# Performance work log

Measured on AMD Instinct MI355X. Metric: run time of the kernel, lower is better.

The kernel has to match this reference:

```python
import jax, jax.numpy as jnp
import numpy as np

N, T, S = 8192, 512, 4
ND, NC = 8, 16


def setup_inputs() -> dict:
    key = jax.random.key(0)
    ks = jax.random.split(key, 8)
    return {
        "drivers": jax.random.normal(ks[0], (N, T, ND), jnp.float32),
        "covariates": jax.random.normal(ks[1], (N, T, NC), jnp.float32),
        "Y": jax.random.normal(ks[2], (N, T, 1), jnp.float32),
        "eps": jax.random.normal(ks[3], (S, N, T, 1), jnp.float32),
        "tilde_psi": jnp.array([0.5], jnp.float32),
        "gamma_w": jax.random.normal(ks[4], (1, ND), jnp.float32) * 0.1,
        "alpha_w": jax.random.normal(ks[5], (1, NC), jnp.float32) * 0.1,
        "alpha_Y_lag": jnp.array([0.1], jnp.float32),
        "log_tilde_sigma": jnp.array([-1.0], jnp.float32),
        "mu_init": jnp.array([0.0], jnp.float32),
        "log_sigma_init": jnp.array([0.0], jnp.float32),
    }


def reference(drivers, covariates, Y, eps, tilde_psi, gamma_w, alpha_w,
              alpha_Y_lag, log_tilde_sigma, mu_init, log_sigma_init):
    psi = tilde_psi[0]
    sigma = jnp.exp(log_tilde_sigma[0])
    sigma0 = jnp.exp(log_sigma_init[0])

    # Structural drift gamma^T D_t + alpha^T W_t for all t in parallel: (N, T)
    proj = (jnp.einsum('ntd,d->nt', drivers, gamma_w[0])
            + jnp.einsum('ntc,c->nt', covariates, alpha_w[0]))
    # b_t for t>=1 includes lagged-outcome term alpha_Y_lag * Y_{t-1}: (N, T-1)
    b = proj[:, 1:] + alpha_Y_lag[0] * Y[:, :-1, 0]

    # Initial step (use_Y_in_init=False): mu_0 = mu_init + proj_0
    mu0 = mu_init[0] + proj[:, 0]                      # (N,)
    e = eps[..., 0]                                    # (S, N, T)
    Z0 = mu0[None, :] + sigma0 * e[:, :, 0]            # (S, N)

    def step(Z, xs):
        b_t, e_t = xs                                  # (N,), (S, N)
        mu_t = psi * Z + b_t[None, :]
        Z_new = mu_t + sigma * e_t
        return Z_new, (Z_new, mu_t)

    xs = (b.T, jnp.moveaxis(e[:, :, 1:], 2, 0))        # (T-1, N), (T-1, S, N)
    _, (Zs, mus) = jax.lax.scan(step, Z0, xs)          # each (T-1, S, N)

    Z_all = jnp.concatenate([Z0[None], Zs], axis=0)    # (T, S, N)
    mu_all = jnp.concatenate([jnp.broadcast_to(mu0, (S, N))[None], mus], axis=0)

    Z_out = jnp.moveaxis(Z_all, 0, 2)[..., None]       # (S, N, T, 1)
    mu_out = jnp.moveaxis(mu_all, 0, 2)[..., None]

    lv0 = jnp.broadcast_to(2.0 * log_sigma_init[0], (S, N, 1))
    lvt = jnp.broadcast_to(2.0 * log_tilde_sigma[0], (S, N, T - 1))
    lv_out = jnp.concatenate([lv0, lvt], axis=2)[..., None]

    return Z_out, mu_out, lv_out
```

## Files before the change

kernel.cpp:

```cpp
#include <hip/hip_runtime.h>

#define N 8192
#define T 512
#define S 4

__device__ __forceinline__ float dot4(float4 a, float4 b) {
    return a.x*b.x + a.y*b.y + a.z*b.z + a.w*b.w;
}

__global__ __launch_bounds__(256) void k_fused(
        const float* __restrict__ drivers,
        const float* __restrict__ cov,
        const float* __restrict__ Y,
        const float* __restrict__ eps,
        const float* __restrict__ tilde_psi,
        const float* __restrict__ gamma_w,
        const float* __restrict__ alpha_w,
        const float* __restrict__ alpha_Y_lag,
        const float* __restrict__ log_tilde_sigma,
        const float* __restrict__ mu_init,
        const float* __restrict__ log_sigma_init,
        float* __restrict__ Zout,
        float* __restrict__ muout,
        float* __restrict__ lvout) {
    const int n    = blockIdx.x * (blockDim.x >> 6) + (threadIdx.x >> 6);
    const int lane = threadIdx.x & 63;
    const int t0   = lane * 8;

    const float psi    = tilde_psi[0];
    const float lts    = log_tilde_sigma[0];
    const float lsi    = log_sigma_init[0];
    const float sigma  = expf(lts);
    const float sigma0 = expf(lsi);
    const float aY     = alpha_Y_lag[0];

    const float4* g4 = (const float4*)gamma_w;
    const float4* a4 = (const float4*)alpha_w;
    const float4 g0 = g4[0], g1 = g4[1];
    const float4 w0 = a4[0], w1 = a4[1], w2 = a4[2], w3 = a4[3];

    float pj[9];
    pj[0] = 1.f;
    #pragma unroll
    for (int i = 1; i <= 8; ++i) pj[i] = pj[i-1] * psi;
    float wd[6];
    wd[0] = pj[8];
    #pragma unroll
    for (int i = 1; i < 6; ++i) wd[i] = wd[i-1] * wd[i-1];

    const size_t ntbase = (size_t)n * T + t0;
    float b[8];
    {
        float proj[8];
        #pragma unroll
        for (int j = 0; j < 8; ++j) {
            const float4* d4 = (const float4*)(drivers + (ntbase + j) * 8);
            const float4* c4 = (const float4*)(cov     + (ntbase + j) * 16);
            float4 dA = d4[0], dB = d4[1];
            float4 cA = c4[0], cB = c4[1], cC = c4[2], cD = c4[3];
            proj[j] = dot4(dA, g0) + dot4(dB, g1)
                    + dot4(cA, w0) + dot4(cB, w1) + dot4(cC, w2) + dot4(cD, w3);
        }
        const float4* y4 = (const float4*)(Y + ntbase);
        float4 yA = y4[0], yB = y4[1];
        float yprev = __shfl_up(yB.w, 1);
        b[0] = (lane == 0) ? (mu_init[0] + proj[0]) : (proj[0] + aY * yprev);
        b[1] = proj[1] + aY * yA.x;
        b[2] = proj[2] + aY * yA.y;
        b[3] = proj[3] + aY * yA.z;
        b[4] = proj[4] + aY * yA.w;
        b[5] = proj[5] + aY * yB.x;
        b[6] = proj[6] + aY * yB.y;
        b[7] = proj[7] + aY * yB.z;
    }

    const float lvv = 2.f * lts;
    const float4 lB = make_float4(lvv, lvv, lvv, lvv);
    const float4 lA = make_float4(lane == 0 ? 2.f * lsi : lvv, lvv, lvv, lvv);

    #pragma unroll
    for (int s = 0; s < S; ++s) {
        const size_t chain = ((size_t)s * N + n) * T + t0;
        const float4* e4 = (const float4*)(eps + chain);
        float4 eA = e4[0], eB = e4[1];
        float e[8] = {eA.x, eA.y, eA.z, eA.w, eB.x, eB.y, eB.z, eB.w};

        float z[8];
        float acc = 0.f;
        #pragma unroll
        for (int j = 0; j < 8; ++j) {
            float sg = (lane == 0 && j == 0) ? sigma0 : sigma;
            acc = psi * acc + (b[j] + sg * e[j]);
            z[j] = acc;
        }

        float v = acc;
        #pragma unroll
        for (int i = 0, d = 1; d < 64; d <<= 1, ++i) {
            float up = __shfl_up(v, d);
            v += (lane >= d) ? wd[i] * up : 0.f;
        }
        float Zprev = __shfl_up(v, 1);
        Zprev = (lane == 0) ? 0.f : Zprev;

        float Zf[8], mu[8];
        #pragma unroll
        for (int j = 0; j < 8; ++j) {
            Zf[j] = z[j] + pj[j + 1] * Zprev;
            float sg = (lane == 0 && j == 0) ? sigma0 : sigma;
            mu[j] = Zf[j] - sg * e[j];
        }

        float4* z4 = (float4*)(Zout  + chain);
        float4* m4 = (float4*)(muout + chain);
        float4* l4 = (float4*)(lvout + chain);
        z4[0] = make_float4(Zf[0], Zf[1], Zf[2], Zf[3]);
        z4[1] = make_float4(Zf[4], Zf[5], Zf[6], Zf[7]);
        m4[0] = make_float4(mu[0], mu[1], mu[2], mu[3]);
        m4[1] = make_float4(mu[4], mu[5], mu[6], mu[7]);
        l4[0] = lA;
        l4[1] = lB;
    }
}

extern "C" void kernel_launch(void* const* d_in, const int* in_sizes, int n_in,
                              void* d_out, int out_size, void* d_ws, size_t ws_size,
                              hipStream_t stream) {
    const float* drivers   = (const float*)d_in[0];
    const float* cov       = (const float*)d_in[1];
    const float* Y         = (const float*)d_in[2];
    const float* eps       = (const float*)d_in[3];
    const float* tilde_psi = (const float*)d_in[4];
    const float* gamma_w   = (const float*)d_in[5];
    const float* alpha_w   = (const float*)d_in[6];
    const float* aY        = (const float*)d_in[7];
    const float* lts       = (const float*)d_in[8];
    const float* mu_init   = (const float*)d_in[9];
    const float* lsi       = (const float*)d_in[10];

    float* out   = (float*)d_out;
    const size_t SNT = (size_t)S * N * T;
    float* Zout  = out;
    float* muout = out + SNT;
    float* lvout = out + 2 * SNT;

    k_fused<<<N / 4, 256, 0, stream>>>(drivers, cov, Y, eps, tilde_psi,
                                       gamma_w, alpha_w, aY, lts, mu_init, lsi,
                                       Zout, muout, lvout);
}
```

Measured before the change: 154.3 us.

## Stage driver/covariate rows through swizzled LDS and map one wave per sample

Each block now handles a single series n. All 256 threads first load that series' drivers and covariates with fully coalesced float4 reads into XOR-swizzled shared memory, then compute the drift b into shared memory. Each wave then runs one of the S=4 chains as two 256-step segments, doing a wave scan on 4 elements per lane and carrying the tail value between segments. This replaces per-lane strided 8-row loads and removes the duplicated eps/output work per series. In exchange it adds block barriers and shared-memory traffic and launches 4x more blocks.

```diff
diff --git a/kernel.cpp b/kernel.cpp
--- a/kernel.cpp
+++ b/kernel.cpp
@@ -7,6 +7,7 @@
 __device__ __forceinline__ float dot4(float4 a, float4 b) {
     return a.x*b.x + a.y*b.y + a.z*b.z + a.w*b.w;
 }
+__device__ __forceinline__ int swz(int c) { return c ^ ((c >> 3) & 7); }
 
 __global__ __launch_bounds__(256) void k_fused(
         const float* __restrict__ drivers,
@@ -23,9 +24,15 @@
         float* __restrict__ Zout,
         float* __restrict__ muout,
         float* __restrict__ lvout) {
-    const int n    = blockIdx.x * (blockDim.x >> 6) + (threadIdx.x >> 6);
-    const int lane = threadIdx.x & 63;
-    const int t0   = lane * 8;
+    __shared__ float4 dstage[512];
+    __shared__ float4 cstage[1024];
+    __shared__ float4 b_s4[128];
+    float* b_s = (float*)b_s4;
+
+    const int tid  = threadIdx.x;
+    const int lane = tid & 63;
+    const int w    = tid >> 6;
+    const int n    = blockIdx.x;
 
     const float psi    = tilde_psi[0];
     const float lts    = log_tilde_sigma[0];
@@ -33,93 +40,106 @@
     const float sigma  = expf(lts);
     const float sigma0 = expf(lsi);
     const float aY     = alpha_Y_lag[0];
+    const float mu0c   = mu_init[0];
 
     const float4* g4 = (const float4*)gamma_w;
     const float4* a4 = (const float4*)alpha_w;
     const float4 g0 = g4[0], g1 = g4[1];
     const float4 w0 = a4[0], w1 = a4[1], w2 = a4[2], w3 = a4[3];
 
-    float pj[9];
-    pj[0] = 1.f;
+    const size_t chain = ((size_t)w * N + n) * (T / 4);
+    const float4* e4 = (const float4*)eps + chain;
+    const float4 eA = e4[lane];
+    const float4 eB = e4[64 + lane];
+
+    const float4* drv4 = (const float4*)drivers + (size_t)n * (T * 2);
+    const float4* cov4 = (const float4*)cov     + (size_t)n * (T * 4);
+    const float*  Yrow = Y + (size_t)n * T;
+
     #pragma unroll
-    for (int i = 1; i <= 8; ++i) pj[i] = pj[i-1] * psi;
-    float wd[6];
-    wd[0] = pj[8];
-    #pragma unroll
-    for (int i = 1; i < 6; ++i) wd[i] = wd[i-1] * wd[i-1];
+    for (int h = 0; h < 2; ++h) {
+        if (h) __syncthreads();
+        dstage[swz(tid)]       = drv4[h * 512 + tid];
+        dstage[swz(tid + 256)] = drv4[h * 512 + 256 + tid];
+        #pragma unroll
+        for (int k = 0; k < 4; ++k)
+            cstage[swz(tid + 256 * k)] = cov4[h * 1024 + tid + 256 * k];
+        const int t = h * 256 + tid;
+        const float yprev = (t > 0) ? Yrow[t - 1] : 0.f;
+        __syncthreads();
+        const float4 dA = dstage[swz(2 * tid)];
+        const float4 dB = dstage[swz(2 * tid + 1)];
+        const float4 cA = cstage[swz(4 * tid)];
+        const float4 cB = cstage[swz(4 * tid + 1)];
+        const float4 cC = cstage[swz(4 * tid + 2)];
+        const float4 cD = cstage[swz(4 * tid + 3)];
+        const float proj = dot4(dA, g0) + dot4(dB, g1)
+                         + dot4(cA, w0) + dot4(cB, w1)
+                         + dot4(cC, w2) + dot4(cD, w3);
+        b_s[t] = (t == 0) ? (mu0c + proj) : (proj + aY * yprev);
+    }
+    __syncthreads();
 
-    const size_t ntbase = (size_t)n * T + t0;
-    float b[8];
+    const float pj1 = psi, pj2 = psi * psi, pj3 = pj2 * psi, pj4 = pj2 * pj2;
+    const float wd0 = pj4, wd1 = wd0 * wd0, wd2 = wd1 * wd1,
+                wd3 = wd2 * wd2, wd4 = wd3 * wd3, wd5 = wd4 * wd4;
+    float p4l = 1.f;
     {
-        float proj[8];
-        #pragma unroll
-        for (int j = 0; j < 8; ++j) {
-            const float4* d4 = (const float4*)(drivers + (ntbase + j) * 8);
-            const float4* c4 = (const float4*)(cov     + (ntbase + j) * 16);
-            float4 dA = d4[0], dB = d4[1];
-            float4 cA = c4[0], cB = c4[1], cC = c4[2], cD = c4[3];
-            proj[j] = dot4(dA, g0) + dot4(dB, g1)
-                    + dot4(cA, w0) + dot4(cB, w1) + dot4(cC, w2) + dot4(cD, w3);
-        }
-        const float4* y4 = (const float4*)(Y + ntbase);
-        float4 yA = y4[0], yB = y4[1];
-        float yprev = __shfl_up(yB.w, 1);
-        b[0] = (lane == 0) ? (mu_init[0] + proj[0]) : (proj[0] + aY * yprev);
-        b[1] = proj[1] + aY * yA.x;
-        b[2] = proj[2] + aY * yA.y;
-        b[3] = proj[3] + aY * yA.z;
-        b[4] = proj[4] + aY * yA.w;
-        b[5] = proj[5] + aY * yB.x;
-        b[6] = proj[6] + aY * yB.y;
-        b[7] = proj[7] + aY * yB.z;
+        float pw = pj4;
+        p4l *= (lane & 1)  ? pw : 1.f; pw *= pw;
+        p4l *= (lane & 2)  ? pw : 1.f; pw *= pw;
+        p4l *= (lane & 4)  ? pw : 1.f; pw *= pw;
+        p4l *= (lane & 8)  ? pw : 1.f; pw *= pw;
+        p4l *= (lane & 16) ? pw : 1.f; pw *= pw;
+        p4l *= (lane & 32) ? pw : 1.f;
     }
 
+    float4* z4 = (float4*)Zout  + chain;
+    float4* m4 = (float4*)muout + chain;
+    float4* l4 = (float4*)lvout + chain;
     const float lvv = 2.f * lts;
-    const float4 lB = make_float4(lvv, lvv, lvv, lvv);
-    const float4 lA = make_float4(lane == 0 ? 2.f * lsi : lvv, lvv, lvv, lvv);
 
+    float Zlast = 0.f;
     #pragma unroll
-    for (int s = 0; s < S; ++s) {
-        const size_t chain = ((size_t)s * N + n) * T + t0;
-        const float4* e4 = (const float4*)(eps + chain);
-        float4 eA = e4[0], eB = e4[1];
-        float e[8] = {eA.x, eA.y, eA.z, eA.w, eB.x, eB.y, eB.z, eB.w};
+    for (int seg = 0; seg < 2; ++seg) {
+        const float4 e  = seg ? eB : eA;
+        const float4 bq = b_s4[seg * 64 + lane];
 
-        float z[8];
-        float acc = 0.f;
-        #pragma unroll
-        for (int j = 0; j < 8; ++j) {
-            float sg = (lane == 0 && j == 0) ? sigma0 : sigma;
-            acc = psi * acc + (b[j] + sg * e[j]);
-            z[j] = acc;
-        }
+        const float sg0 = (seg == 0 && lane == 0) ? sigma0 : sigma;
+        const float z0 = bq.x + sg0 * e.x;
+        const float z1 = psi * z0 + (bq.y + sigma * e.y);
+        const float z2 = psi * z1 + (bq.z + sigma * e.z);
+        const float z3 = psi * z2 + (bq.w + sigma * e.w);
 
-        float v = acc;
-        #pragma unroll
-        for (int i = 0, d = 1; d < 64; d <<= 1, ++i) {
-            float up = __shfl_up(v, d);
-            v += (lane >= d) ? wd[i] * up : 0.f;
-        }
+        float v = z3, up;
+        up = __shfl_up(v, 1);  v += (lane >= 1)  ? wd0 * up : 0.f;
+        up = __shfl_up(v, 2);  v += (lane >= 2)  ? wd1 * up : 0.f;
+        up = __shfl_up(v, 4);  v += (lane >= 4)  ? wd2 * up : 0.f;
+        up = __shfl_up(v, 8);  v += (lane >= 8)  ? wd3 * up : 0.f;
+        up = __shfl_up(v, 16); v += (lane >= 16) ? wd4 * up : 0.f;
+        up = __shfl_up(v, 32); v += (lane >= 32) ? wd5 * up : 0.f;
+
         float Zprev = __shfl_up(v, 1);
         Zprev = (lane == 0) ? 0.f : Zprev;
+        Zprev += p4l * Zlast;
 
-        float Zf[8], mu[8];
-        #pragma unroll
-        for (int j = 0; j < 8; ++j) {
-            Zf[j] = z[j] + pj[j + 1] * Zprev;
-            float sg = (lane == 0 && j == 0) ? sigma0 : sigma;
-            mu[j] = Zf[j] - sg * e[j];
-        }
+        const float Z0 = z0 + pj1 * Zprev;
+        const float Z1 = z1 + pj2 * Zprev;
+        const float Z2 = z2 + pj3 * Zprev;
+        const float Z3 = z3 + pj4 * Zprev;
 
-        float4* z4 = (float4*)(Zout  + chain);
-        float4* m4 = (float4*)(muout + chain);
-        float4* l4 = (float4*)(lvout + chain);
-        z4[0] = make_float4(Zf[0], Zf[1], Zf[2], Zf[3]);
-        z4[1] = make_float4(Zf[4], Zf[5], Zf[6], Zf[7]);
-        m4[0] = make_float4(mu[0], mu[1], mu[2], mu[3]);
-        m4[1] = make_float4(mu[4], mu[5], mu[6], mu[7]);
-        l4[0] = lA;
-        l4[1] = lB;
+        const float mu0 = Z0 - sg0   * e.x;
+        const float mu1 = Z1 - sigma * e.y;
+        const float mu2 = Z2 - sigma * e.z;
+        const float mu3 = Z3 - sigma * e.w;
+
+        z4[seg * 64 + lane] = make_float4(Z0, Z1, Z2, Z3);
+        m4[seg * 64 + lane] = make_float4(mu0, mu1, mu2, mu3);
+        l4[seg * 64 + lane] = (seg == 0 && lane == 0)
+                            ? make_float4(2.f * lsi, lvv, lvv, lvv)
+                            : make_float4(lvv, lvv, lvv, lvv);
+
+        Zlast = __shfl(Z3, 63);
     }
 }
 
@@ -144,7 +164,7 @@
     float* muout = out + SNT;
     float* lvout = out + 2 * SNT;
 
-    k_fused<<<N / 4, 256, 0, stream>>>(drivers, cov, Y, eps, tilde_psi,
-                                       gamma_w, alpha_w, aY, lts, mu_init, lsi,
-                                       Zout, muout, lvout);
+    k_fused<<<N, 256, 0, stream>>>(drivers, cov, Y, eps, tilde_psi,
+                                   gamma_w, alpha_w, aY, lts, mu_init, lsi,
+                                   Zout, muout, lvout);
 }
```

New measurement: 140.9 us. 8.7% less time.
